# Performance work log

Hardware: AMD Instinct MI355X
Metric: run time of the kernel (lower is better)

Reference implementation:

```python
import jax, jax.numpy as jnp
import numpy as np

IN_F = 4096
OUT_F = 4096
GS = 128  # group_size


def setup_inputs() -> dict:
    key = jax.random.key(0)
    k1, k2, k3 = jax.random.split(key, 3)
    x = jax.random.normal(k1, (4, 2048, IN_F), dtype=jnp.float32)
    # ternary codes in {-1, 0, 1}, stored as int8 in the original module
    ternary = jax.random.randint(k2, (OUT_F, IN_F), 0, 3, dtype=jnp.int32) - 1
    ternary = ternary.astype(jnp.int8)
    n_groups = OUT_F * IN_F // GS
    # per-group positive scales (abs-mean init in original); keep them O(1e-2)
    scales = jax.random.uniform(k3, (n_groups,), dtype=jnp.float32, minval=0.005, maxval=0.05)
    return {"x": x, "ternary": ternary, "scales": scales}


def reference(x, ternary, scales):
    # Reconstruct full-precision weight: each contiguous group of GS elements
    # (row-major over [out, in]) shares one scale.
    w = ternary.astype(jnp.float32).reshape(-1, GS) * scales[:, None]
    w = w.reshape(OUT_F, IN_F)
    # F.linear(x, w) == x @ w.T
    return jnp.einsum("bsd,od->bso", x, w)
```

## Files before the change

kernel.cpp:

```cpp
#include <hip/hip_runtime.h>


typedef __attribute__((ext_vector_type(8))) short      bf16x8;
typedef __attribute__((ext_vector_type(4))) float      f32x4;
typedef __attribute__((ext_vector_type(8))) float      f32x8;
typedef __attribute__((ext_vector_type(8))) unsigned short u16x8;
typedef __attribute__((ext_vector_type(4))) int        i32x4;

#define M_DIM 8192
#define N_DIM 4096
#define K_DIM 4096
#define BM 128
#define BN 128
#define BK 32

__device__ __forceinline__ unsigned short f2bf(float f) {
  union { float f; unsigned u; } v; v.f = f;
  unsigned u = v.u;
  u += 0x7FFFu + ((u >> 16) & 1u);
  return (unsigned short)(u >> 16);
}

__global__ void cvt_x_kernel(const float* __restrict__ x,
                             unsigned short* __restrict__ y, int n8) {
  int stride = gridDim.x * blockDim.x;
  for (int i = blockIdx.x * blockDim.x + threadIdx.x; i < n8; i += stride) {
    f32x8 f = ((const f32x8*)x)[i];
    u16x8 o;
#pragma unroll
    for (int j = 0; j < 8; ++j) o[j] = f2bf(f[j]);
    ((u16x8*)y)[i] = o;
  }
}

__global__ void cvt_w_kernel(const int* __restrict__ t, const float* __restrict__ s,
                             unsigned short* __restrict__ w, int n8) {
  int stride = gridDim.x * blockDim.x;
  for (int i = blockIdx.x * blockDim.x + threadIdx.x; i < n8; i += stride) {
    i32x4 a = ((const i32x4*)t)[2 * i + 0];
    i32x4 b = ((const i32x4*)t)[2 * i + 1];
    float sc = s[i >> 4];
    u16x8 o;
    o[0] = f2bf((float)a[0] * sc);
    o[1] = f2bf((float)a[1] * sc);
    o[2] = f2bf((float)a[2] * sc);
    o[3] = f2bf((float)a[3] * sc);
    o[4] = f2bf((float)b[0] * sc);
    o[5] = f2bf((float)b[1] * sc);
    o[6] = f2bf((float)b[2] * sc);
    o[7] = f2bf((float)b[3] * sc);
    ((u16x8*)w)[i] = o;
  }
}

__global__ void gemm_bt_kernel(const unsigned short* __restrict__ A,
                               const unsigned short* __restrict__ B,
                               float* __restrict__ C) {
  __shared__ __align__(16) unsigned short sA[BM * BK];
  __shared__ __align__(16) unsigned short sB[BN * BK];

  const int tid  = threadIdx.x;
  const int lane = tid & 63;
  const int wave = tid >> 6;
  const int wm = wave >> 1;
  const int wn = wave & 1;

  const int nwg = gridDim.x;
  const int cpx = nwg >> 3;
  const int wg  = (blockIdx.x & 7) * cpx + (blockIdx.x >> 3);
  const int nN  = N_DIM / BN;
  const int bm  = wg / nN;
  const int bn  = wg % nN;

  const unsigned short* Ab = A + (size_t)bm * BM * K_DIM;
  const unsigned short* Bb = B + (size_t)bn * BN * K_DIM;

  const int ga0 = (tid >> 2) * K_DIM + (tid & 3) * 8;
  const int ga1 = ga0 + 64 * K_DIM;

  const f32x4 fzero = {0.f, 0.f, 0.f, 0.f};
  f32x4 acc[4][4];
#pragma unroll
  for (int mr = 0; mr < 4; ++mr)
#pragma unroll
    for (int nr = 0; nr < 4; ++nr) acc[mr][nr] = fzero;

  const int r  = lane & 15;
  const int kq = lane >> 4;

  for (int k0 = 0; k0 < K_DIM; k0 += BK) {
    __builtin_amdgcn_global_load_lds(
        (const __attribute__((address_space(1))) void*)(Ab + ga0 + k0),
        (__attribute__((address_space(3))) void*)(sA + wave * 512), 16, 0, 0);
    __builtin_amdgcn_global_load_lds(
        (const __attribute__((address_space(1))) void*)(Ab + ga1 + k0),
        (__attribute__((address_space(3))) void*)(sA + 2048 + wave * 512), 16, 0, 0);
    __builtin_amdgcn_global_load_lds(
        (const __attribute__((address_space(1))) void*)(Bb + ga0 + k0),
        (__attribute__((address_space(3))) void*)(sB + wave * 512), 16, 0, 0);
    __builtin_amdgcn_global_load_lds(
        (const __attribute__((address_space(1))) void*)(Bb + ga1 + k0),
        (__attribute__((address_space(3))) void*)(sB + 2048 + wave * 512), 16, 0, 0);

    __syncthreads();

    bf16x8 af[4], bfr[4];
#pragma unroll
    for (int mr = 0; mr < 4; ++mr)
      af[mr] = *(const bf16x8*)&sA[(wm * 64 + mr * 16 + r) * BK + kq * 8];
#pragma unroll
    for (int nr = 0; nr < 4; ++nr)
      bfr[nr] = *(const bf16x8*)&sB[(wn * 64 + nr * 16 + r) * BK + kq * 8];

#pragma unroll
    for (int mr = 0; mr < 4; ++mr)
#pragma unroll
      for (int nr = 0; nr < 4; ++nr)
        acc[mr][nr] = __builtin_amdgcn_mfma_f32_16x16x32_bf16(
            af[mr], bfr[nr], acc[mr][nr], 0, 0, 0);

    __syncthreads();
  }

  const int row0 = bm * BM + wm * 64 + (lane >> 4) * 4;
  const int col0 = bn * BN + wn * 64 + (lane & 15);
#pragma unroll
  for (int mr = 0; mr < 4; ++mr) {
#pragma unroll
    for (int nr = 0; nr < 4; ++nr) {
#pragma unroll
      for (int j = 0; j < 4; ++j) {
        C[(size_t)(row0 + mr * 16 + j) * N_DIM + (col0 + nr * 16)] = acc[mr][nr][j];
      }
    }
  }
}

extern "C" void kernel_launch(void* const* d_in, const int* in_sizes, int n_in,
                              void* d_out, int out_size, void* d_ws, size_t ws_size,
                              hipStream_t stream) {
  const float* x      = (const float*)d_in[0];
  const int*   tern   = (const int*)d_in[1];
  const float* scales = (const float*)d_in[2];
  float* out = (float*)d_out;

  unsigned short* xb = (unsigned short*)d_ws;
  unsigned short* wb = (unsigned short*)d_ws + (size_t)M_DIM * K_DIM;

  cvt_x_kernel<<<2048, 256, 0, stream>>>(x, xb, M_DIM * K_DIM / 8);
  cvt_w_kernel<<<2048, 256, 0, stream>>>(tern, scales, wb, N_DIM * K_DIM / 8);

  const int grid = (M_DIM / BM) * (N_DIM / BN);
  gemm_bt_kernel<<<grid, 256, 0, stream>>>(xb, wb, out);
}
```

Measured before the change: 599.3 us.

## Replace GEMM with 256x256 double-buffered, swizzled, interleaved-prefetch MFMA kernel

Replaces the 128x128x32 single-buffered GEMM with a 256x256x64 tile kernel using 8 waves, 128 KB of dynamic LDS split into two buffers, and XOR-swizzled LDS layout. Global-to-LDS loads for the next K-tile are interleaved with four MFMA phases per iteration, using explicit waitcnt, barriers and setprio to overlap memory with compute. The goals are higher arithmetic intensity per block, fewer LDS bank conflicts, and hidden load latency. The cost is larger register and LDS footprint, which limits occupancy, and more complex synchronisation that is easy to get wrong.

```diff
diff --git a/kernel.cpp b/kernel.cpp
--- a/kernel.cpp
+++ b/kernel.cpp
@@ -10,9 +10,11 @@
 #define M_DIM 8192
 #define N_DIM 4096
 #define K_DIM 4096
-#define BM 128
-#define BN 128
-#define BK 32
+#define BM 256
+#define BN 256
+#define BK 64
+#define NT (K_DIM / BK)
+#define THREADS 512
 
 __device__ __forceinline__ unsigned short f2bf(float f) {
   union { float f; unsigned u; } v; v.f = f;
@@ -41,99 +43,177 @@
     i32x4 b = ((const i32x4*)t)[2 * i + 1];
     float sc = s[i >> 4];
     u16x8 o;
-    o[0] = f2bf((float)a[0] * sc);
-    o[1] = f2bf((float)a[1] * sc);
-    o[2] = f2bf((float)a[2] * sc);
-    o[3] = f2bf((float)a[3] * sc);
-    o[4] = f2bf((float)b[0] * sc);
-    o[5] = f2bf((float)b[1] * sc);
-    o[6] = f2bf((float)b[2] * sc);
-    o[7] = f2bf((float)b[3] * sc);
+    o[0] = f2bf((float)a[0] * sc); o[1] = f2bf((float)a[1] * sc);
+    o[2] = f2bf((float)a[2] * sc); o[3] = f2bf((float)a[3] * sc);
+    o[4] = f2bf((float)b[0] * sc); o[5] = f2bf((float)b[1] * sc);
+    o[6] = f2bf((float)b[2] * sc); o[7] = f2bf((float)b[3] * sc);
     ((u16x8*)w)[i] = o;
   }
 }
 
-__global__ void gemm_bt_kernel(const unsigned short* __restrict__ A,
-                               const unsigned short* __restrict__ B,
-                               float* __restrict__ C) {
-  __shared__ __align__(16) unsigned short sA[BM * BK];
-  __shared__ __align__(16) unsigned short sB[BN * BK];
+__global__ __launch_bounds__(THREADS, 2)
+void gemm256_kernel(const unsigned short* __restrict__ A,
+                    const unsigned short* __restrict__ B,
+                    float* __restrict__ C) {
+  extern __shared__ char smem[];
 
   const int tid  = threadIdx.x;
   const int lane = tid & 63;
   const int wave = tid >> 6;
-  const int wm = wave >> 1;
-  const int wn = wave & 1;
-
-  const int nwg = gridDim.x;
-  const int cpx = nwg >> 3;
-  const int wg  = (blockIdx.x & 7) * cpx + (blockIdx.x >> 3);
-  const int nN  = N_DIM / BN;
-  const int bm  = wg / nN;
-  const int bn  = wg % nN;
-
-  const unsigned short* Ab = A + (size_t)bm * BM * K_DIM;
-  const unsigned short* Bb = B + (size_t)bn * BN * K_DIM;
-
-  const int ga0 = (tid >> 2) * K_DIM + (tid & 3) * 8;
-  const int ga1 = ga0 + 64 * K_DIM;
+  const int wm   = wave >> 2;
+  const int wn   = wave & 3;
+
+  const int blk = blockIdx.x;
+  const int wg  = (blk & 7) * (512 / 8) + (blk >> 3);
+  const int bm  = wg >> 4;
+  const int bn  = wg & 15;
+
+  const int srow = tid >> 3;
+  const int scol = 8 * ((tid & 7) ^ (srow & 7));
+  const unsigned short* Ap = A + (size_t)(bm * BM + srow) * K_DIM + scol;
+  const unsigned short* Bp = B + (size_t)(bn * BN + srow) * K_DIM + scol;
+  const int ldsWave = wave * 1024;
+
+  auto STAGE = [&](int c, int ab, int T, int j) {
+    const unsigned short* src =
+        (ab == 0 ? Ap : Bp) + (size_t)j * 64 * K_DIM + (size_t)T * BK;
+    char* dst = smem + c * 65536 + ab * 32768 + j * 8192 + ldsWave;
+    __builtin_amdgcn_global_load_lds(
+        (const __attribute__((address_space(1))) void*)src,
+        (__attribute__((address_space(3))) void*)dst, 16, 0, 0);
+  };
+
+  const int r   = lane & 15;
+  const int kq  = lane >> 4;
+  const int swz = (lane & 7) << 3;
+  auto RD_A = [&](int c, int mf, int ks) -> bf16x8 {
+    const int row = wm * 128 + mf * 16 + r;
+    const int col = (ks * 32 + kq * 8) ^ swz;
+    return *(const bf16x8*)(smem + c * 65536 + (row * 64 + col) * 2);
+  };
+  auto RD_B = [&](int c, int nf, int ks) -> bf16x8 {
+    const int row = wn * 64 + nf * 16 + r;
+    const int col = (ks * 32 + kq * 8) ^ swz;
+    return *(const bf16x8*)(smem + c * 65536 + 32768 + (row * 64 + col) * 2);
+  };
 
   const f32x4 fzero = {0.f, 0.f, 0.f, 0.f};
-  f32x4 acc[4][4];
-#pragma unroll
-  for (int mr = 0; mr < 4; ++mr)
-#pragma unroll
-    for (int nr = 0; nr < 4; ++nr) acc[mr][nr] = fzero;
-
-  const int r  = lane & 15;
-  const int kq = lane >> 4;
-
-  for (int k0 = 0; k0 < K_DIM; k0 += BK) {
-    __builtin_amdgcn_global_load_lds(
-        (const __attribute__((address_space(1))) void*)(Ab + ga0 + k0),
-        (__attribute__((address_space(3))) void*)(sA + wave * 512), 16, 0, 0);
-    __builtin_amdgcn_global_load_lds(
-        (const __attribute__((address_space(1))) void*)(Ab + ga1 + k0),
-        (__attribute__((address_space(3))) void*)(sA + 2048 + wave * 512), 16, 0, 0);
-    __builtin_amdgcn_global_load_lds(
-        (const __attribute__((address_space(1))) void*)(Bb + ga0 + k0),
-        (__attribute__((address_space(3))) void*)(sB + wave * 512), 16, 0, 0);
-    __builtin_amdgcn_global_load_lds(
-        (const __attribute__((address_space(1))) void*)(Bb + ga1 + k0),
-        (__attribute__((address_space(3))) void*)(sB + 2048 + wave * 512), 16, 0, 0);
-
-    __syncthreads();
-
-    bf16x8 af[4], bfr[4];
-#pragma unroll
-    for (int mr = 0; mr < 4; ++mr)
-      af[mr] = *(const bf16x8*)&sA[(wm * 64 + mr * 16 + r) * BK + kq * 8];
-#pragma unroll
-    for (int nr = 0; nr < 4; ++nr)
-      bfr[nr] = *(const bf16x8*)&sB[(wn * 64 + nr * 16 + r) * BK + kq * 8];
-
-#pragma unroll
-    for (int mr = 0; mr < 4; ++mr)
-#pragma unroll
-      for (int nr = 0; nr < 4; ++nr)
-        acc[mr][nr] = __builtin_amdgcn_mfma_f32_16x16x32_bf16(
-            af[mr], bfr[nr], acc[mr][nr], 0, 0, 0);
-
-    __syncthreads();
+  f32x4 acc[8][4];
+#pragma unroll
+  for (int mf = 0; mf < 8; ++mf)
+#pragma unroll
+    for (int nf = 0; nf < 4; ++nf) acc[mf][nf] = fzero;
+
+#pragma unroll
+  for (int j = 0; j < 4; ++j) STAGE(0, 0, 0, j);
+#pragma unroll
+  for (int j = 0; j < 4; ++j) STAGE(0, 1, 0, j);
+#pragma unroll
+  for (int j = 0; j < 4; ++j) STAGE(1, 1, 1, j);
+  asm volatile("s_waitcnt vmcnt(4)" ::: "memory");
+  __builtin_amdgcn_s_barrier();
+
+  for (int t = 0; t < NT; ++t) {
+    const int cur = t & 1;
+    const int nxt = cur ^ 1;
+    bf16x8 aLo[4][2], aHi[4][2], bF[4][2];
+
+#pragma unroll
+    for (int mf = 0; mf < 4; ++mf)
+#pragma unroll
+      for (int ks = 0; ks < 2; ++ks) aLo[mf][ks] = RD_A(cur, mf, ks);
+#pragma unroll
+    for (int nf = 0; nf < 2; ++nf)
+#pragma unroll
+      for (int ks = 0; ks < 2; ++ks) bF[nf][ks] = RD_B(cur, nf, ks);
+    if (t + 1 < NT) { STAGE(nxt, 0, t + 1, 0); STAGE(nxt, 0, t + 1, 1); }
+    __builtin_amdgcn_s_barrier();
+    asm volatile("s_waitcnt lgkmcnt(0)" ::: "memory");
+    __builtin_amdgcn_sched_barrier(0);
+    __builtin_amdgcn_s_setprio(1);
+#pragma unroll
+    for (int mf = 0; mf < 4; ++mf)
+#pragma unroll
+      for (int nf = 0; nf < 2; ++nf)
+#pragma unroll
+        for (int ks = 0; ks < 2; ++ks)
+          acc[mf][nf] = __builtin_amdgcn_mfma_f32_16x16x32_bf16(
+              aLo[mf][ks], bF[nf][ks], acc[mf][nf], 0, 0, 0);
+    __builtin_amdgcn_s_setprio(0);
+    __builtin_amdgcn_s_barrier();
+
+#pragma unroll
+    for (int nf = 2; nf < 4; ++nf)
+#pragma unroll
+      for (int ks = 0; ks < 2; ++ks) bF[nf][ks] = RD_B(cur, nf, ks);
+    if (t + 1 < NT) { STAGE(nxt, 0, t + 1, 2); STAGE(nxt, 0, t + 1, 3); }
+    __builtin_amdgcn_s_barrier();
+    asm volatile("s_waitcnt lgkmcnt(0)" ::: "memory");
+    __builtin_amdgcn_sched_barrier(0);
+    __builtin_amdgcn_s_setprio(1);
+#pragma unroll
+    for (int mf = 0; mf < 4; ++mf)
+#pragma unroll
+      for (int nf = 2; nf < 4; ++nf)
+#pragma unroll
+        for (int ks = 0; ks < 2; ++ks)
+          acc[mf][nf] = __builtin_amdgcn_mfma_f32_16x16x32_bf16(
+              aLo[mf][ks], bF[nf][ks], acc[mf][nf], 0, 0, 0);
+    __builtin_amdgcn_s_setprio(0);
+    __builtin_amdgcn_s_barrier();
+
+#pragma unroll
+    for (int mf = 0; mf < 4; ++mf)
+#pragma unroll
+      for (int ks = 0; ks < 2; ++ks) aHi[mf][ks] = RD_A(cur, mf + 4, ks);
+    if (t + 2 < NT) { STAGE(cur, 1, t + 2, 0); STAGE(cur, 1, t + 2, 1); }
+    __builtin_amdgcn_s_barrier();
+    asm volatile("s_waitcnt lgkmcnt(0)" ::: "memory");
+    __builtin_amdgcn_sched_barrier(0);
+    __builtin_amdgcn_s_setprio(1);
+#pragma unroll
+    for (int mf = 0; mf < 4; ++mf)
+#pragma unroll
+      for (int nf = 0; nf < 2; ++nf)
+#pragma unroll
+        for (int ks = 0; ks < 2; ++ks)
+          acc[mf + 4][nf] = __builtin_amdgcn_mfma_f32_16x16x32_bf16(
+              aHi[mf][ks], bF[nf][ks], acc[mf + 4][nf], 0, 0, 0);
+    __builtin_amdgcn_s_setprio(0);
+    __builtin_amdgcn_s_barrier();
+
+    if (t + 2 < NT) { STAGE(cur, 1, t + 2, 2); STAGE(cur, 1, t + 2, 3); }
+    __builtin_amdgcn_s_barrier();
+    __builtin_amdgcn_s_setprio(1);
+#pragma unroll
+    for (int mf = 0; mf < 4; ++mf)
+#pragma unroll
+      for (int nf = 2; nf < 4; ++nf)
+#pragma unroll
+        for (int ks = 0; ks < 2; ++ks)
+          acc[mf + 4][nf] = __builtin_amdgcn_mfma_f32_16x16x32_bf16(
+              aHi[mf][ks], bF[nf][ks], acc[mf + 4][nf], 0, 0, 0);
+    __builtin_amdgcn_s_setprio(0);
+    if (t + 2 < NT) {
+      asm volatile("s_waitcnt vmcnt(4)" ::: "memory");
+    } else if (t + 1 < NT) {
+      asm volatile("s_waitcnt vmcnt(0)" ::: "memory");
+    }
+    __builtin_amdgcn_s_barrier();
   }
 
-  const int row0 = bm * BM + wm * 64 + (lane >> 4) * 4;
-  const int col0 = bn * BN + wn * 64 + (lane & 15);
-#pragma unroll
-  for (int mr = 0; mr < 4; ++mr) {
-#pragma unroll
-    for (int nr = 0; nr < 4; ++nr) {
-#pragma unroll
-      for (int j = 0; j < 4; ++j) {
-        C[(size_t)(row0 + mr * 16 + j) * N_DIM + (col0 + nr * 16)] = acc[mr][nr][j];
-      }
-    }
-  }
+  const int r4 = (lane >> 4) * 4;
+  const int cc = lane & 15;
+  const size_t row0 = (size_t)bm * BM + wm * 128;
+  const size_t col0 = (size_t)bn * BN + wn * 64;
+#pragma unroll
+  for (int mf = 0; mf < 8; ++mf)
+#pragma unroll
+    for (int nf = 0; nf < 4; ++nf)
+#pragma unroll
+      for (int j = 0; j < 4; ++j)
+        C[(row0 + mf * 16 + r4 + j) * N_DIM + col0 + nf * 16 + cc] =
+            acc[mf][nf][j];
 }
 
 extern "C" void kernel_launch(void* const* d_in, const int* in_sizes, int n_in,
@@ -150,6 +230,8 @@
   cvt_x_kernel<<<2048, 256, 0, stream>>>(x, xb, M_DIM * K_DIM / 8);
   cvt_w_kernel<<<2048, 256, 0, stream>>>(tern, scales, wb, N_DIM * K_DIM / 8);
 
+  hipFuncSetAttribute((const void*)gemm256_kernel,
+                      hipFuncAttributeMaxDynamicSharedMemorySize, 131072);
   const int grid = (M_DIM / BM) * (N_DIM / BN);
-  gemm_bt_kernel<<<grid, 256, 0, stream>>>(xb, wb, out);
-}
+  gemm256_kernel<<<grid, THREADS, 131072, stream>>>(xb, wb, out);
+}
```

Result: faster. 488.0 us (-18.6%).
